# Kernel tuning notes

Hardware: AMD Instinct MI355X
Metric: run time of the kernel (lower is better)

The kernel has to match this reference:

```python
import jax, jax.numpy as jnp
import numpy as np
from jax import lax

D, DIM, FF, V, B, S = 8, 1024, 4096, 32000, 2, 2048
EPS = 1e-6

def _rms(x, w):
    return x * lax.rsqrt(jnp.mean(x * x, axis=-1, keepdims=True) + EPS) * w

def _lin(x, W, b):
    # torch nn.Linear: weight [out, in]
    return x @ W.T + b

def _comb(e1, e2):
    # associative op for h_t = a_t * h_{t-1} + b_t  (h_0 = 0)
    a1, b1 = e1
    a2, b2 = e2
    return a1 * a2, a2 * b1 + b2

def _forward(tokens, emb, h0, Wf, bf, Wi, bi, Wig, big, Wog, bog, n1, n2, Wfc, bfc, Wfa, bfa, Wfo, bfo, nl, Wout, bout):
    # embedding with max_norm=1 renorm semantics
    e = emb[tokens]                                  # [B,S,DIM]
    nrm = jnp.linalg.norm(e, axis=-1, keepdims=True)
    x = jnp.where(nrm > 1.0, e / (nrm + 1e-7), e)
    for i in range(D):
        # --- QuasiLSTM sub-block ---
        x_ = x
        h_in = _rms(x, n1[i])
        f = jax.nn.sigmoid(_lin(h_in, Wf[i], bf[i]))                 # forget gate [B,S,DIM]
        v = jnp.tanh(_lin(h_in, Wi[i], bi[i])) * jax.nn.sigmoid(_lin(h_in, Wig[i], big[i]))
        _, h_inner = lax.associative_scan(_comb, (f, v), axis=1)     # inner-chunk scan (zero init)
        h = h_inner + h0[i][None, None, :] * jnp.cumprod(f, axis=1)  # cross-chunk from last_hidden_init
        y = jnp.tanh(h) * jax.nn.sigmoid(_lin(h_in, Wog[i], bog[i]))
        x = y + x_                                                   # dropout(p) is identity in eval
        # --- SwiGLU FFN sub-block ---
        x_ = x
        z = _rms(x, n2[i])
        u = _lin(z, Wfc[i], bfc[i]) * jax.nn.silu(_lin(z, Wfa[i], bfa[i]))
        x = _lin(u, Wfo[i], bfo[i]) + x_
    x = _rms(x, nl)
    return _lin(x, Wout, bout)                                       # [B,S,V]

def setup_inputs() -> dict:
    key = jax.random.key(0)
    ks = jax.random.split(key, 16)
    n = lambda k, s: jax.random.normal(k, s, jnp.float32) * 0.02
    zD = jnp.zeros((D, DIM), jnp.float32)
    return {
        "tokens": jax.random.randint(ks[0], (B, S), 0, V),
        "emb": n(ks[1], (V, DIM)),
        "h0": jax.random.normal(ks[2], (D, DIM), jnp.float32),
        "Wf": n(ks[3], (D, DIM, DIM)), "bf": zD,
        "Wi": n(ks[4], (D, DIM, DIM)), "bi": zD,
        "Wig": n(ks[5], (D, DIM, DIM)), "big": zD,
        "Wog": n(ks[6], (D, DIM, DIM)), "bog": zD,
        "n1": jnp.ones((D, DIM), jnp.float32),
        "n2": jnp.ones((D, DIM), jnp.float32),
        "Wfc": n(ks[7], (D, FF, DIM)), "bfc": jnp.zeros((D, FF), jnp.float32),
        "Wfa": n(ks[8], (D, FF, DIM)), "bfa": jnp.zeros((D, FF), jnp.float32),
        "Wfo": n(ks[9], (D, DIM, FF)), "bfo": zD,
        "nl": jnp.ones((DIM,), jnp.float32),
        "Wout": n(ks[10], (V, DIM)), "bout": jnp.zeros((V,), jnp.float32),
    }

def reference(tokens, emb, h0, Wf, bf, Wi, bi, Wig, big, Wog, bog, n1, n2, Wfc, bfc, Wfa, bfa, Wfo, bfo, nl, Wout, bout):
    return _forward(tokens, emb, h0, Wf, bf, Wi, bi, Wig, big, Wog, bog, n1, n2, Wfc, bfc, Wfa, bfa, Wfo, bfo, nl, Wout, bout)
```

## Files before the change

### kernel.cpp

```cpp
#include <hip/hip_runtime.h>
#include <hip/hip_bf16.h>
#include <cstdint>
#include <cstddef>

typedef unsigned short u16;
typedef __attribute__((ext_vector_type(4))) float f32x4;
typedef __attribute__((ext_vector_type(8))) short bf16x8;
typedef __attribute__((ext_vector_type(8))) unsigned short u16x8;
typedef __attribute__((ext_vector_type(4))) unsigned short u16x4;

#define D_LAYERS 8
#define DIMN 1024
#define FFD 4096
#define VOCAB 32000
#define MROWS 4096
#define SEQ 2048
#define NCHUNK 64
#define LCHUNK 32

__device__ __forceinline__ u16 f2b(float f) {
  union { float f; unsigned u; } v; v.f = f;
  unsigned r = v.u + 0x7FFFu + ((v.u >> 16) & 1u);
  return (u16)(r >> 16);
}
__device__ __forceinline__ float b2f(u16 h) {
  union { unsigned u; float f; } v; v.u = ((unsigned)h) << 16;
  return v.f;
}
__device__ __forceinline__ float sigm(float x) { return 1.f / (1.f + __expf(-x)); }

__device__ __forceinline__ void async16(const void* g, void* l) {
  auto gp = reinterpret_cast<const __attribute__((address_space(1))) char*>(
      reinterpret_cast<uintptr_t>(g));
  auto lp = reinterpret_cast<__attribute__((address_space(3))) char*>(
      reinterpret_cast<uintptr_t>(l));
  __builtin_amdgcn_global_load_lds(gp, lp, 16, 0, 0);
}

__device__ __forceinline__ float blk_sum(float v) {
  __shared__ float sm[4];
  #pragma unroll
  for (int o = 32; o > 0; o >>= 1) v += __shfl_xor(v, o);
  if ((threadIdx.x & 63) == 0) sm[threadIdx.x >> 6] = v;
  __syncthreads();
  float r = sm[0] + sm[1] + sm[2] + sm[3];
  __syncthreads();
  return r;
}

__global__ __launch_bounds__(256) void k_cvt(const f32x4* __restrict__ in,
                                             u16x8* __restrict__ out) {
  size_t i = (size_t)blockIdx.x * 256 + threadIdx.x;
  f32x4 a = in[i * 2], b = in[i * 2 + 1];
  u16x8 o;
  o[0] = f2b(a[0]); o[1] = f2b(a[1]); o[2] = f2b(a[2]); o[3] = f2b(a[3]);
  o[4] = f2b(b[0]); o[5] = f2b(b[1]); o[6] = f2b(b[2]); o[7] = f2b(b[3]);
  out[i] = o;
}

__global__ __launch_bounds__(256) void k_embed(const int* __restrict__ tok,
                                               const float* __restrict__ emb,
                                               float* __restrict__ x) {
  const int r = blockIdx.x;
  const int tk = tok[r];
  f32x4 v = ((const f32x4*)(emb + (size_t)tk * DIMN))[threadIdx.x];
  float ss = v[0]*v[0] + v[1]*v[1] + v[2]*v[2] + v[3]*v[3];
  float tot = blk_sum(ss);
  float nrm = sqrtf(tot);
  float s = (nrm > 1.f) ? (1.f / (nrm + 1e-7f)) : 1.f;
  f32x4 o = {v[0]*s, v[1]*s, v[2]*s, v[3]*s};
  ((f32x4*)(x + (size_t)r * DIMN))[threadIdx.x] = o;
}

__global__ __launch_bounds__(256) void k_rms(const float* __restrict__ x,
                                             const float* __restrict__ wgt,
                                             u16* __restrict__ out) {
  const int r = blockIdx.x;
  f32x4 v = ((const f32x4*)(x + (size_t)r * DIMN))[threadIdx.x];
  float ss = v[0]*v[0] + v[1]*v[1] + v[2]*v[2] + v[3]*v[3];
  float tot = blk_sum(ss);
  float sc = rsqrtf(tot * (1.f / DIMN) + 1e-6f);
  f32x4 w = ((const f32x4*)wgt)[threadIdx.x];
  u16x4 o;
  o[0] = f2b(v[0] * sc * w[0]);
  o[1] = f2b(v[1] * sc * w[1]);
  o[2] = f2b(v[2] * sc * w[2]);
  o[3] = f2b(v[3] * sc * w[3]);
  ((u16x4*)(out + (size_t)r * DIMN))[threadIdx.x] = o;
}

__global__ __launch_bounds__(256) void k_scanA(const float* __restrict__ f,
                                               const float* __restrict__ ti,
                                               const float* __restrict__ gg,
                                               float* __restrict__ Ac,
                                               float* __restrict__ Vc) {
  const int bx = blockIdx.x;
  const int dg = bx & 3, c = (bx >> 2) & 63, b = bx >> 8;
  const int d = dg * 256 + threadIdx.x;
  const size_t base = ((size_t)(b * SEQ + c * LCHUNK)) * DIMN + d;
  float a = 1.f, h = 0.f;
  #pragma unroll 4
  for (int t = 0; t < LCHUNK; ++t) {
    size_t ix = base + (size_t)t * DIMN;
    float fv = f[ix];
    float vv = ti[ix] * gg[ix];
    h = fv * h + vv;
    a *= fv;
  }
  const size_t ci = ((size_t)(b * NCHUNK + c)) * DIMN + d;
  Ac[ci] = a; Vc[ci] = h;
}

__global__ __launch_bounds__(256) void k_scanB(const float* __restrict__ Ac,
                                               const float* __restrict__ Vc,
                                               const float* __restrict__ h0,
                                               float* __restrict__ carry) {
  const int idx = blockIdx.x * 256 + threadIdx.x;
  const int b = idx >> 10, d = idx & 1023;
  float h = h0[d];
  for (int c = 0; c < NCHUNK; ++c) {
    size_t ci = ((size_t)(b * NCHUNK + c)) * DIMN + d;
    carry[ci] = h;
    h = Ac[ci] * h + Vc[ci];
  }
}

__global__ __launch_bounds__(256) void k_scanC(const float* __restrict__ f,
                                               const float* __restrict__ ti,
                                               const float* __restrict__ gg,
                                               const float* __restrict__ oo,
                                               const float* __restrict__ carry,
                                               float* __restrict__ x) {
  const int bx = blockIdx.x;
  const int dg = bx & 3, c = (bx >> 2) & 63, b = bx >> 8;
  const int d = dg * 256 + threadIdx.x;
  const size_t base = ((size_t)(b * SEQ + c * LCHUNK)) * DIMN + d;
  float h = carry[((size_t)(b * NCHUNK + c)) * DIMN + d];
  for (int t = 0; t < LCHUNK; ++t) {
    size_t ix = base + (size_t)t * DIMN;
    float fv = f[ix];
    h = fv * h + ti[ix] * gg[ix];
    float y = tanhf(h) * oo[ix];
    x[ix] += y;
  }
}

constexpr int EPI_GATES = 0, EPI_SILU_BF = 1, EPI_MUL_BF = 2, EPI_RES_F32 = 3,
              EPI_BIAS_F32 = 4;

template<int BN_T, int EPI>
__global__ __launch_bounds__(256, 2)
void gemm_bt(const u16* __restrict__ A,
             const u16* __restrict__ B0, const u16* __restrict__ B1,
             const u16* __restrict__ B2, const u16* __restrict__ B3,
             const float* __restrict__ bias0, const float* __restrict__ bias1,
             const float* __restrict__ bias2, const float* __restrict__ bias3,
             float* __restrict__ oF0, float* __restrict__ oF1,
             float* __restrict__ oF2, float* __restrict__ oF3,
             u16* __restrict__ oB,
             const u16* __restrict__ exB, const float* __restrict__ exF,
             int N, int K)
{
  constexpr int MF = (BN_T == 128) ? 4 : 2;
  constexpr int WAVES_N = (BN_T == 128) ? 2 : 1;
  constexpr int ISS_B = BN_T / 32;
  __shared__ __align__(16) u16 As[128 * 64];
  __shared__ __align__(16) u16 Bs[BN_T * 64];
  const int tid = threadIdx.x;
  const int w = tid >> 6, lane = tid & 63;
  const int wm = w / WAVES_N, wn = w % WAVES_N;
  const int m0 = blockIdx.x * 128;
  const int n0 = blockIdx.y * BN_T;
  const int z = blockIdx.z;

  const u16* Bw;
  const float* bias;
  float* oF;
  if constexpr (EPI == EPI_GATES) {
    Bw   = (z == 0) ? B0 : (z == 1) ? B1 : (z == 2) ? B2 : B3;
    bias = (z == 0) ? bias0 : (z == 1) ? bias1 : (z == 2) ? bias2 : bias3;
    oF   = (z == 0) ? oF0 : (z == 1) ? oF1 : (z == 2) ? oF2 : oF3;
  } else {
    Bw = B0; bias = bias0; oF = oF0;
  }

  const f32x4 zero = {0.f, 0.f, 0.f, 0.f};
  f32x4 acc[MF][4];
  #pragma unroll
  for (int mf = 0; mf < MF; ++mf)
    #pragma unroll
    for (int nf = 0; nf < 4; ++nf) acc[mf][nf] = zero;

  for (int kt = 0; kt < K; kt += 64) {
    #pragma unroll
    for (int i = 0; i < 4; ++i) {
      int p = i * 4096 + w * 1024 + lane * 16;
      int r = p >> 7;
      int cs = (p & 127) ^ ((r & 7) << 4);
      async16(A + ((size_t)(m0 + r) * K + kt) + (cs >> 1),
              (char*)As + i * 4096 + w * 1024);
    }
    #pragma unroll
    for (int i = 0; i < ISS_B; ++i) {
      int p = i * 4096 + w * 1024 + lane * 16;
      int r = p >> 7;
      int cs = (p & 127) ^ ((r & 7) << 4);
      async16(Bw + ((size_t)(n0 + r) * K + kt) + (cs >> 1),
              (char*)Bs + i * 4096 + w * 1024);
    }
    __syncthreads();
    #pragma unroll
    for (int ks = 0; ks < 2; ++ks) {
      bf16x8 av[MF], bv[4];
      const int cbase = ks * 64 + ((lane >> 4) << 4);
      #pragma unroll
      for (int mf = 0; mf < MF; ++mf) {
        int r = wm * (MF * 16) + mf * 16 + (lane & 15);
        av[mf] = *(const bf16x8*)((const char*)As + r * 128 + (cbase ^ ((r & 7) << 4)));
      }
      #pragma unroll
      for (int nf = 0; nf < 4; ++nf) {
        int r = wn * 64 + nf * 16 + (lane & 15);
        bv[nf] = *(const bf16x8*)((const char*)Bs + r * 128 + (cbase ^ ((r & 7) << 4)));
      }
      #pragma unroll
      for (int mf = 0; mf < MF; ++mf)
        #pragma unroll
        for (int nf = 0; nf < 4; ++nf)
          acc[mf][nf] = __builtin_amdgcn_mfma_f32_16x16x32_bf16(
              av[mf], bv[nf], acc[mf][nf], 0, 0, 0);
    }
    __syncthreads();
  }

  #pragma unroll
  for (int nf = 0; nf < 4; ++nf) {
    const int n = n0 + wn * 64 + nf * 16 + (lane & 15);
    const float bb = bias[n];
    #pragma unroll
    for (int mf = 0; mf < MF; ++mf) {
      #pragma unroll
      for (int j = 0; j < 4; ++j) {
        const int m = m0 + wm * (MF * 16) + mf * 16 + ((lane >> 4) << 2) + j;
        const size_t idx = (size_t)m * N + n;
        float v = acc[mf][nf][j] + bb;
        if constexpr (EPI == EPI_GATES) {
          oF[idx] = (z == 1) ? tanhf(v) : sigm(v);
        } else if constexpr (EPI == EPI_SILU_BF) {
          oB[idx] = f2b(v * sigm(v));
        } else if constexpr (EPI == EPI_MUL_BF) {
          oB[idx] = f2b(v * b2f(exB[idx]));
        } else if constexpr (EPI == EPI_RES_F32) {
          oF[idx] = v + exF[idx];
        } else {
          oF[idx] = v;
        }
      }
    }
  }
}

extern "C" void kernel_launch(void* const* d_in, const int* in_sizes, int n_in,
                              void* d_out, int out_size, void* d_ws, size_t ws_size,
                              hipStream_t stream) {
  (void)in_sizes; (void)n_in; (void)out_size; (void)ws_size;
  const int*   tokens = (const int*)d_in[0];
  const float* emb  = (const float*)d_in[1];
  const float* h0   = (const float*)d_in[2];
  const float* Wf   = (const float*)d_in[3];
  const float* bf_  = (const float*)d_in[4];
  const float* Wi   = (const float*)d_in[5];
  const float* bi_  = (const float*)d_in[6];
  const float* Wig  = (const float*)d_in[7];
  const float* big_ = (const float*)d_in[8];
  const float* Wog  = (const float*)d_in[9];
  const float* bog_ = (const float*)d_in[10];
  const float* n1   = (const float*)d_in[11];
  const float* n2   = (const float*)d_in[12];
  const float* Wfc  = (const float*)d_in[13];
  const float* bfc_ = (const float*)d_in[14];
  const float* Wfa  = (const float*)d_in[15];
  const float* bfa_ = (const float*)d_in[16];
  const float* Wfo  = (const float*)d_in[17];
  const float* bfo_ = (const float*)d_in[18];
  const float* nl_  = (const float*)d_in[19];
  const float* Wout = (const float*)d_in[20];
  const float* bout_= (const float*)d_in[21];
  float* out = (float*)d_out;

  char* p = (char*)d_ws;
  auto alloc = [&](size_t bytes) {
    char* r = p; p += (bytes + 255) & ~(size_t)255; return r;
  };
  u16* wbWf   = (u16*)alloc((size_t)DIMN * DIMN * 2);
  u16* wbWi   = (u16*)alloc((size_t)DIMN * DIMN * 2);
  u16* wbWig  = (u16*)alloc((size_t)DIMN * DIMN * 2);
  u16* wbWog  = (u16*)alloc((size_t)DIMN * DIMN * 2);
  u16* wbWfc  = (u16*)alloc((size_t)FFD * DIMN * 2);
  u16* wbWfa  = (u16*)alloc((size_t)FFD * DIMN * 2);
  u16* wbWfo  = (u16*)alloc((size_t)FFD * DIMN * 2);
  u16* wbWout = (u16*)alloc((size_t)VOCAB * DIMN * 2);
  float* x    = (float*)alloc((size_t)MROWS * DIMN * 4);
  u16* hin    = (u16*)alloc((size_t)MROWS * DIMN * 2);
  float* fbuf = (float*)alloc((size_t)MROWS * DIMN * 4);
  float* tibuf= (float*)alloc((size_t)MROWS * DIMN * 4);
  float* ggbuf= (float*)alloc((size_t)MROWS * DIMN * 4);
  float* oobuf= (float*)alloc((size_t)MROWS * DIMN * 4);
  u16* sa = (u16*)fbuf;
  u16* ub = (u16*)((char*)fbuf + (size_t)MROWS * FFD * 2);
  float* Ac    = (float*)alloc((size_t)2 * NCHUNK * DIMN * 4);
  float* Vc    = (float*)alloc((size_t)2 * NCHUNK * DIMN * 4);
  float* carry = (float*)alloc((size_t)2 * NCHUNK * DIMN * 4);

  auto cvt = [&](const float* src, u16* dst, size_t nelem) {
    k_cvt<<<dim3((unsigned)(nelem / 2048)), dim3(256), 0, stream>>>(
        (const f32x4*)src, (u16x8*)dst);
  };

  k_embed<<<dim3(MROWS), dim3(256), 0, stream>>>(tokens, emb, x);

  for (int L = 0; L < D_LAYERS; ++L) {
    const size_t oDD = (size_t)L * DIMN * DIMN;
    const size_t oFD = (size_t)L * FFD * DIMN;
    cvt(Wf  + oDD, wbWf,  (size_t)DIMN * DIMN);
    cvt(Wi  + oDD, wbWi,  (size_t)DIMN * DIMN);
    cvt(Wig + oDD, wbWig, (size_t)DIMN * DIMN);
    cvt(Wog + oDD, wbWog, (size_t)DIMN * DIMN);
    cvt(Wfc + oFD, wbWfc, (size_t)FFD * DIMN);
    cvt(Wfa + oFD, wbWfa, (size_t)FFD * DIMN);
    cvt(Wfo + oFD, wbWfo, (size_t)FFD * DIMN);

    k_rms<<<dim3(MROWS), dim3(256), 0, stream>>>(x, n1 + (size_t)L * DIMN, hin);

    gemm_bt<128, EPI_GATES><<<dim3(32, 8, 4), dim3(256), 0, stream>>>(
        hin, wbWf, wbWi, wbWig, wbWog,
        bf_ + (size_t)L * DIMN, bi_ + (size_t)L * DIMN,
        big_ + (size_t)L * DIMN, bog_ + (size_t)L * DIMN,
        fbuf, tibuf, ggbuf, oobuf,
        nullptr, nullptr, nullptr, DIMN, DIMN);

    k_scanA<<<dim3(512), dim3(256), 0, stream>>>(fbuf, tibuf, ggbuf, Ac, Vc);
    k_scanB<<<dim3(8), dim3(256), 0, stream>>>(Ac, Vc, h0 + (size_t)L * DIMN, carry);
    k_scanC<<<dim3(512), dim3(256), 0, stream>>>(fbuf, tibuf, ggbuf, oobuf, carry, x);

    k_rms<<<dim3(MROWS), dim3(256), 0, stream>>>(x, n2 + (size_t)L * DIMN, hin);

    gemm_bt<128, EPI_SILU_BF><<<dim3(32, 32, 1), dim3(256), 0, stream>>>(
        hin, wbWfa, nullptr, nullptr, nullptr,
        bfa_ + (size_t)L * FFD, nullptr, nullptr, nullptr,
        nullptr, nullptr, nullptr, nullptr,
        sa, nullptr, nullptr, FFD, DIMN);

    gemm_bt<128, EPI_MUL_BF><<<dim3(32, 32, 1), dim3(256), 0, stream>>>(
        hin, wbWfc, nullptr, nullptr, nullptr,
        bfc_ + (size_t)L * FFD, nullptr, nullptr, nullptr,
        nullptr, nullptr, nullptr, nullptr,
        ub, sa, nullptr, FFD, DIMN);

    gemm_bt<64, EPI_RES_F32><<<dim3(32, 16, 1), dim3(256), 0, stream>>>(
        ub, wbWfo, nullptr, nullptr, nullptr,
        bfo_ + (size_t)L * DIMN, nullptr, nullptr, nullptr,
        x, nullptr, nullptr, nullptr,
        nullptr, nullptr, x, DIMN, FFD);
  }

  cvt(Wout, wbWout, (size_t)VOCAB * DIMN);
  k_rms<<<dim3(MROWS), dim3(256), 0, stream>>>(x, nl_, hin);
  gemm_bt<128, EPI_BIAS_F32><<<dim3(32, 250, 1), dim3(256), 0, stream>>>(
      hin, wbWout, nullptr, nullptr, nullptr,
      bout_, nullptr, nullptr, nullptr,
      out, nullptr, nullptr, nullptr,
      nullptr, nullptr, nullptr, VOCAB, DIMN);
}
```

Baseline: 2.518 ms.

## Add 256x256 double-buffered MFMA GEMM for gates, FFN-up and vocab projections

Introduces a new 512-thread GEMM kernel with 256x256 output tiles and a 128KB double-buffered LDS stage loaded by async copies. It uses a swizzled LDS layout and interleaves loads with MFMA quarter-steps under barriers and priority hints. The four gate weights are packed contiguously so a single N=4096 GEMM computes all gates. The FFN up/gate and vocab GEMMs use the new kernel, and the FFN down GEMM tile is changed from 64 to 128. Larger tiles are meant to raise data reuse and MFMA utilization, at the cost of high LDS use that limits each CU to one block and fewer blocks for the smaller GEMMs.

Result: slower. 2.974 ms (+18.1%).

```diff
diff --git a/kernel.cpp b/kernel.cpp
--- a/kernel.cpp
+++ b/kernel.cpp
@@ -256,6 +256,173 @@
           oF[idx] = v;
         }
       }
+    }
+  }
+}
+
+constexpr int EG4 = 0, ESILU = 1, EMUL = 2, EVOC = 3;
+
+template<int EPI>
+__global__ __launch_bounds__(512, 2)
+void gemm256(const u16* __restrict__ A, const u16* __restrict__ Bm,
+             const float* __restrict__ b0, const float* __restrict__ b1,
+             const float* __restrict__ b2, const float* __restrict__ b3,
+             float* __restrict__ f0, float* __restrict__ f1,
+             float* __restrict__ f2, float* __restrict__ f3,
+             u16* __restrict__ oB, const u16* __restrict__ exB,
+             float* __restrict__ oF,
+             int N, int K, int GX)
+{
+  __shared__ __align__(16) char lds[131072];
+  const int tid = threadIdx.x;
+  const int w = tid >> 6, lane = tid & 63;
+  const int wm = w >> 2, wn = w & 3;
+  const int nwg = gridDim.x, bid = blockIdx.x;
+  const int swz = (bid & 7) * (nwg >> 3) + (bid >> 3);
+  const int m0 = (swz % GX) * 256;
+  const int n0 = (swz / GX) * 256;
+
+  int Dj[8];
+  #pragma unroll
+  for (int j = 0; j < 6; ++j) {
+    const int e = w * 6 + j;
+    Dj[j] = (e < 32) ? (32768 + (e << 10))
+                     : ((((e - 32) >> 3) << 14) + (((e - 32) & 7) << 10));
+  }
+  #pragma unroll
+  for (int j = 0; j < 2; ++j) {
+    const int l = (w << 1) + j;
+    Dj[6 + j] = ((l >> 3) << 14) + 8192 + ((l & 7) << 10);
+  }
+
+  auto issue = [&](int buf, int j, int kt) {
+    const int d = Dj[j];
+    const int qq = d + (lane << 4);
+    const int row = (qq & 32767) >> 7;
+    const int cs = (qq & 127) ^ ((row & 7) << 4);
+    const u16* src = (qq >> 15)
+        ? (Bm + ((size_t)(n0 + row) * K + kt) + (cs >> 1))
+        : (A  + ((size_t)(m0 + row) * K + kt) + (cs >> 1));
+    async16(src, lds + (buf << 16) + d);
+  };
+  auto rdA = [&](int buf, int mf, int ks) -> bf16x8 {
+    const int row = wm * 128 + mf * 16 + (lane & 15);
+    const int col = (ks * 64 + ((lane >> 4) << 4)) ^ ((row & 7) << 4);
+    return *(const bf16x8*)(lds + (buf << 16) + row * 128 + col);
+  };
+  auto rdB = [&](int buf, int nf, int ks) -> bf16x8 {
+    const int row = wn * 64 + nf * 16 + (lane & 15);
+    const int col = (ks * 64 + ((lane >> 4) << 4)) ^ ((row & 7) << 4);
+    return *(const bf16x8*)(lds + (buf << 16) + 32768 + row * 128 + col);
+  };
+
+  const f32x4 zero = {0.f, 0.f, 0.f, 0.f};
+  f32x4 acc[8][4];
+  #pragma unroll
+  for (int mf = 0; mf < 8; ++mf)
+    #pragma unroll
+    for (int nf = 0; nf < 4; ++nf) acc[mf][nf] = zero;
+  bf16x8 av[4][2], bv[2][2];
+
+#define MM256(MFO, NFO)                                                    \
+  __builtin_amdgcn_s_setprio(1);                                           \
+  _Pragma("unroll")                                                        \
+  for (int mf = 0; mf < 4; ++mf)                                           \
+    _Pragma("unroll")                                                      \
+    for (int nf = 0; nf < 2; ++nf)                                         \
+      _Pragma("unroll")                                                    \
+      for (int ks = 0; ks < 2; ++ks)                                       \
+        acc[(MFO) + mf][(NFO) + nf] = __builtin_amdgcn_mfma_f32_16x16x32_bf16( \
+            av[mf][ks], bv[nf][ks], acc[(MFO) + mf][(NFO) + nf], 0, 0, 0); \
+  __builtin_amdgcn_s_setprio(0);
+
+  const int NT = K >> 6;
+  #pragma unroll
+  for (int j = 0; j < 8; ++j) issue(0, j, 0);
+  asm volatile("s_waitcnt vmcnt(2)" ::: "memory");
+  __builtin_amdgcn_s_barrier();
+
+  for (int t = 0; t < NT; ++t) {
+    const int buf = t & 1, nbuf = buf ^ 1;
+    const bool pf = (t + 1 < NT);
+    const int kn = (t + 1) << 6;
+
+    #pragma unroll
+    for (int mf = 0; mf < 4; ++mf) { av[mf][0] = rdA(buf, mf, 0); av[mf][1] = rdA(buf, mf, 1); }
+    #pragma unroll
+    for (int nf = 0; nf < 2; ++nf) { bv[nf][0] = rdB(buf, nf, 0); bv[nf][1] = rdB(buf, nf, 1); }
+    if (pf) { issue(nbuf, 0, kn); issue(nbuf, 1, kn); }
+    __builtin_amdgcn_s_barrier();
+    asm volatile("s_waitcnt lgkmcnt(0)" ::: "memory");
+    MM256(0, 0)
+    __builtin_amdgcn_s_barrier();
+
+    #pragma unroll
+    for (int nf = 0; nf < 2; ++nf) { bv[nf][0] = rdB(buf, 2 + nf, 0); bv[nf][1] = rdB(buf, 2 + nf, 1); }
+    if (pf) { issue(nbuf, 2, kn); issue(nbuf, 3, kn); }
+    __builtin_amdgcn_s_barrier();
+    asm volatile("s_waitcnt lgkmcnt(0)" ::: "memory");
+    MM256(0, 2)
+    if (pf) asm volatile("s_waitcnt vmcnt(4)" ::: "memory");
+    else    asm volatile("s_waitcnt vmcnt(0)" ::: "memory");
+    __builtin_amdgcn_s_barrier();
+
+    #pragma unroll
+    for (int mf = 0; mf < 4; ++mf) { av[mf][0] = rdA(buf, 4 + mf, 0); av[mf][1] = rdA(buf, 4 + mf, 1); }
+    if (pf) { issue(nbuf, 4, kn); issue(nbuf, 5, kn); }
+    __builtin_amdgcn_s_barrier();
+    asm volatile("s_waitcnt lgkmcnt(0)" ::: "memory");
+    MM256(4, 2)
+    __builtin_amdgcn_s_barrier();
+
+    #pragma unroll
+    for (int nf = 0; nf < 2; ++nf) { bv[nf][0] = rdB(buf, nf, 0); bv[nf][1] = rdB(buf, nf, 1); }
+    if (pf) { issue(nbuf, 6, kn); issue(nbuf, 7, kn); }
+    __builtin_amdgcn_s_barrier();
+    asm volatile("s_waitcnt lgkmcnt(0)" ::: "memory");
+    MM256(4, 0)
+    if (pf) asm volatile("s_waitcnt vmcnt(2)" ::: "memory");
+    __builtin_amdgcn_s_barrier();
+  }
+#undef MM256
+
+  if constexpr (EPI == EG4) {
+    const int z = n0 >> 10;
+    const float* bz = (z == 0) ? b0 : (z == 1) ? b1 : (z == 2) ? b2 : b3;
+    float* fz = (z == 0) ? f0 : (z == 1) ? f1 : (z == 2) ? f2 : f3;
+    #pragma unroll
+    for (int nf = 0; nf < 4; ++nf) {
+      const int n = (n0 & 1023) + wn * 64 + nf * 16 + (lane & 15);
+      const float bb = bz[n];
+      #pragma unroll
+      for (int mf = 0; mf < 8; ++mf)
+        #pragma unroll
+        for (int j = 0; j < 4; ++j) {
+          const int m = m0 + wm * 128 + mf * 16 + ((lane >> 4) << 2) + j;
+          float v = acc[mf][nf][j] + bb;
+          fz[(size_t)m * 1024 + n] = (z == 1) ? tanhf(v) : sigm(v);
+        }
+    }
+  } else {
+    #pragma unroll
+    for (int nf = 0; nf < 4; ++nf) {
+      const int n = n0 + wn * 64 + nf * 16 + (lane & 15);
+      const float bb = b0[n];
+      #pragma unroll
+      for (int mf = 0; mf < 8; ++mf)
+        #pragma unroll
+        for (int j = 0; j < 4; ++j) {
+          const int m = m0 + wm * 128 + mf * 16 + ((lane >> 4) << 2) + j;
+          const size_t idx = (size_t)m * N + n;
+          float v = acc[mf][nf][j] + bb;
+          if constexpr (EPI == ESILU) {
+            oB[idx] = f2b(v * sigm(v));
+          } else if constexpr (EPI == EMUL) {
+            oB[idx] = f2b(v * b2f(exB[idx]));
+          } else {
+            oF[idx] = v;
+          }
+        }
     }
   }
 }
@@ -292,10 +459,7 @@
   auto alloc = [&](size_t bytes) {
     char* r = p; p += (bytes + 255) & ~(size_t)255; return r;
   };
-  u16* wbWf   = (u16*)alloc((size_t)DIMN * DIMN * 2);
-  u16* wbWi   = (u16*)alloc((size_t)DIMN * DIMN * 2);
-  u16* wbWig  = (u16*)alloc((size_t)DIMN * DIMN * 2);
-  u16* wbWog  = (u16*)alloc((size_t)DIMN * DIMN * 2);
+  u16* wbGates = (u16*)alloc((size_t)4 * DIMN * DIMN * 2);
   u16* wbWfc  = (u16*)alloc((size_t)FFD * DIMN * 2);
   u16* wbWfa  = (u16*)alloc((size_t)FFD * DIMN * 2);
   u16* wbWfo  = (u16*)alloc((size_t)FFD * DIMN * 2);
@@ -322,22 +486,22 @@
   for (int L = 0; L < D_LAYERS; ++L) {
     const size_t oDD = (size_t)L * DIMN * DIMN;
     const size_t oFD = (size_t)L * FFD * DIMN;
-    cvt(Wf  + oDD, wbWf,  (size_t)DIMN * DIMN);
-    cvt(Wi  + oDD, wbWi,  (size_t)DIMN * DIMN);
-    cvt(Wig + oDD, wbWig, (size_t)DIMN * DIMN);
-    cvt(Wog + oDD, wbWog, (size_t)DIMN * DIMN);
+    cvt(Wf  + oDD, wbGates + (size_t)0 * DIMN * DIMN, (size_t)DIMN * DIMN);
+    cvt(Wi  + oDD, wbGates + (size_t)1 * DIMN * DIMN, (size_t)DIMN * DIMN);
+    cvt(Wig + oDD, wbGates + (size_t)2 * DIMN * DIMN, (size_t)DIMN * DIMN);
+    cvt(Wog + oDD, wbGates + (size_t)3 * DIMN * DIMN, (size_t)DIMN * DIMN);
     cvt(Wfc + oFD, wbWfc, (size_t)FFD * DIMN);
     cvt(Wfa + oFD, wbWfa, (size_t)FFD * DIMN);
     cvt(Wfo + oFD, wbWfo, (size_t)FFD * DIMN);
 
     k_rms<<<dim3(MROWS), dim3(256), 0, stream>>>(x, n1 + (size_t)L * DIMN, hin);
 
-    gemm_bt<128, EPI_GATES><<<dim3(32, 8, 4), dim3(256), 0, stream>>>(
-        hin, wbWf, wbWi, wbWig, wbWog,
+    gemm256<EG4><<<dim3(256), dim3(512), 0, stream>>>(
+        hin, wbGates,
         bf_ + (size_t)L * DIMN, bi_ + (size_t)L * DIMN,
         big_ + (size_t)L * DIMN, bog_ + (size_t)L * DIMN,
         fbuf, tibuf, ggbuf, oobuf,
-        nullptr, nullptr, nullptr, DIMN, DIMN);
+        nullptr, nullptr, nullptr, 4096, DIMN, 16);
 
     k_scanA<<<dim3(512), dim3(256), 0, stream>>>(fbuf, tibuf, ggbuf, Ac, Vc);
     k_scanB<<<dim3(8), dim3(256), 0, stream>>>(Ac, Vc, h0 + (size_t)L * DIMN, carry);
@@ -345,19 +509,19 @@
 
     k_rms<<<dim3(MROWS), dim3(256), 0, stream>>>(x, n2 + (size_t)L * DIMN, hin);
 
-    gemm_bt<128, EPI_SILU_BF><<<dim3(32, 32, 1), dim3(256), 0, stream>>>(
-        hin, wbWfa, nullptr, nullptr, nullptr,
+    gemm256<ESILU><<<dim3(256), dim3(512), 0, stream>>>(
+        hin, wbWfa,
         bfa_ + (size_t)L * FFD, nullptr, nullptr, nullptr,
         nullptr, nullptr, nullptr, nullptr,
-        sa, nullptr, nullptr, FFD, DIMN);
-
-    gemm_bt<128, EPI_MUL_BF><<<dim3(32, 32, 1), dim3(256), 0, stream>>>(
-        hin, wbWfc, nullptr, nullptr, nullptr,
+        sa, nullptr, nullptr, FFD, DIMN, 16);
+
+    gemm256<EMUL><<<dim3(256), dim3(512), 0, stream>>>(
+        hin, wbWfc,
         bfc_ + (size_t)L * FFD, nullptr, nullptr, nullptr,
         nullptr, nullptr, nullptr, nullptr,
-        ub, sa, nullptr, FFD, DIMN);
-
-    gemm_bt<64, EPI_RES_F32><<<dim3(32, 16, 1), dim3(256), 0, stream>>>(
+        ub, sa, nullptr, FFD, DIMN, 16);
+
+    gemm_bt<128, EPI_RES_F32><<<dim3(32, 8), dim3(256), 0, stream>>>(
         ub, wbWfo, nullptr, nullptr, nullptr,
         bfo_ + (size_t)L * DIMN, nullptr, nullptr, nullptr,
         x, nullptr, nullptr, nullptr,
@@ -366,9 +530,9 @@
 
   cvt(Wout, wbWout, (size_t)VOCAB * DIMN);
   k_rms<<<dim3(MROWS), dim3(256), 0, stream>>>(x, nl_, hin);
-  gemm_bt<128, EPI_BIAS_F32><<<dim3(32, 250, 1), dim3(256), 0, stream>>>(
-      hin, wbWout, nullptr, nullptr, nullptr,
+  gemm256<EVOC><<<dim3(2000), dim3(512), 0, stream>>>(
+      hin, wbWout,
       bout_, nullptr, nullptr, nullptr,
-      out, nullptr, nullptr, nullptr,
-      nullptr, nullptr, nullptr, VOCAB, DIMN);
-}
+      nullptr, nullptr, nullptr, nullptr,
+      nullptr, nullptr, out, VOCAB, DIMN, 16);
+}
```

## Fuse paired gate and SwiGLU GEMMs into dual-B kernel, batch weight conversions

Applied to the files above, without the earlier changes.

Adds a dual-output GEMM that shares each A tile across two weight matrices. The tanh input and its sigmoid gate are multiplied in the epilogue, so v is written directly and the scan kernels read one buffer instead of two. The SwiGLU gate and up projections are computed together and written as one bf16 product, removing the intermediate silu buffer round trip and one A reread. The seven per-layer weight conversions merge into one launch, and tanh uses a cheaper exp-based form. The dual kernel uses more LDS and accumulator registers, which may reduce occupancy.

New measurement: 2.139 ms. 1.18x faster.

```diff
diff --git a/kernel.cpp b/kernel.cpp
--- a/kernel.cpp
+++ b/kernel.cpp
@@ -28,6 +28,10 @@
   return v.f;
 }
 __device__ __forceinline__ float sigm(float x) { return 1.f / (1.f + __expf(-x)); }
+__device__ __forceinline__ float ftanh(float x) {
+  float e = __expf(2.f * x);
+  return 1.f - 2.f / (e + 1.f);
+}
 
 __device__ __forceinline__ void async16(const void* g, void* l) {
   auto gp = reinterpret_cast<const __attribute__((address_space(1))) char*>(
@@ -56,6 +60,39 @@
   o[0] = f2b(a[0]); o[1] = f2b(a[1]); o[2] = f2b(a[2]); o[3] = f2b(a[3]);
   o[4] = f2b(b[0]); o[5] = f2b(b[1]); o[6] = f2b(b[2]); o[7] = f2b(b[3]);
   out[i] = o;
+}
+
+__global__ __launch_bounds__(256) void k_cvt7(
+    const float* __restrict__ Wf, const float* __restrict__ Wi,
+    const float* __restrict__ Wig, const float* __restrict__ Wog,
+    const float* __restrict__ Wfc, const float* __restrict__ Wfa,
+    const float* __restrict__ Wfo,
+    u16* __restrict__ dGates,
+    u16* __restrict__ dFc, u16* __restrict__ dFa, u16* __restrict__ dFo,
+    int L)
+{
+  const int b = blockIdx.x;
+  const float* src; u16* dst; size_t off;
+  if (b < 2048) {
+    const int g = b >> 9, r = b & 511;
+    const float* s = (g == 0) ? Wf : (g == 1) ? Wi : (g == 2) ? Wig : Wog;
+    src = s + (size_t)L * 1048576;
+    dst = dGates + (size_t)g * 1048576;
+    off = (size_t)r * 2048;
+  } else if (b < 4096) {
+    src = Wfc + (size_t)L * 4194304; dst = dFc; off = (size_t)(b - 2048) * 2048;
+  } else if (b < 6144) {
+    src = Wfa + (size_t)L * 4194304; dst = dFa; off = (size_t)(b - 4096) * 2048;
+  } else {
+    src = Wfo + (size_t)L * 4194304; dst = dFo; off = (size_t)(b - 6144) * 2048;
+  }
+  const size_t i = off + (size_t)threadIdx.x * 8;
+  f32x4 a = *(const f32x4*)(src + i);
+  f32x4 c = *(const f32x4*)(src + i + 4);
+  u16x8 o;
+  o[0] = f2b(a[0]); o[1] = f2b(a[1]); o[2] = f2b(a[2]); o[3] = f2b(a[3]);
+  o[4] = f2b(c[0]); o[5] = f2b(c[1]); o[6] = f2b(c[2]); o[7] = f2b(c[3]);
+  *(u16x8*)(dst + i) = o;
 }
 
 __global__ __launch_bounds__(256) void k_embed(const int* __restrict__ tok,
@@ -90,8 +127,7 @@
 }
 
 __global__ __launch_bounds__(256) void k_scanA(const float* __restrict__ f,
-                                               const float* __restrict__ ti,
-                                               const float* __restrict__ gg,
+                                               const float* __restrict__ v,
                                                float* __restrict__ Ac,
                                                float* __restrict__ Vc) {
   const int bx = blockIdx.x;
@@ -103,8 +139,7 @@
   for (int t = 0; t < LCHUNK; ++t) {
     size_t ix = base + (size_t)t * DIMN;
     float fv = f[ix];
-    float vv = ti[ix] * gg[ix];
-    h = fv * h + vv;
+    h = fv * h + v[ix];
     a *= fv;
   }
   const size_t ci = ((size_t)(b * NCHUNK + c)) * DIMN + d;
@@ -126,8 +161,7 @@
 }
 
 __global__ __launch_bounds__(256) void k_scanC(const float* __restrict__ f,
-                                               const float* __restrict__ ti,
-                                               const float* __restrict__ gg,
+                                               const float* __restrict__ v,
                                                const float* __restrict__ oo,
                                                const float* __restrict__ carry,
                                                float* __restrict__ x) {
@@ -139,24 +173,19 @@
   for (int t = 0; t < LCHUNK; ++t) {
     size_t ix = base + (size_t)t * DIMN;
     float fv = f[ix];
-    h = fv * h + ti[ix] * gg[ix];
-    float y = tanhf(h) * oo[ix];
-    x[ix] += y;
-  }
-}
-
-constexpr int EPI_GATES = 0, EPI_SILU_BF = 1, EPI_MUL_BF = 2, EPI_RES_F32 = 3,
-              EPI_BIAS_F32 = 4;
+    h = fv * h + v[ix];
+    x[ix] += ftanh(h) * oo[ix];
+  }
+}
+
+constexpr int EPI_SILU_BF = 1, EPI_MUL_BF = 2, EPI_RES_F32 = 3, EPI_BIAS_F32 = 4;
 
 template<int BN_T, int EPI>
 __global__ __launch_bounds__(256, 2)
 void gemm_bt(const u16* __restrict__ A,
-             const u16* __restrict__ B0, const u16* __restrict__ B1,
-             const u16* __restrict__ B2, const u16* __restrict__ B3,
-             const float* __restrict__ bias0, const float* __restrict__ bias1,
-             const float* __restrict__ bias2, const float* __restrict__ bias3,
-             float* __restrict__ oF0, float* __restrict__ oF1,
-             float* __restrict__ oF2, float* __restrict__ oF3,
+             const u16* __restrict__ B0,
+             const float* __restrict__ bias0,
+             float* __restrict__ oF0,
              u16* __restrict__ oB,
              const u16* __restrict__ exB, const float* __restrict__ exF,
              int N, int K)
@@ -171,18 +200,10 @@
   const int wm = w / WAVES_N, wn = w % WAVES_N;
   const int m0 = blockIdx.x * 128;
   const int n0 = blockIdx.y * BN_T;
-  const int z = blockIdx.z;
-
-  const u16* Bw;
-  const float* bias;
-  float* oF;
-  if constexpr (EPI == EPI_GATES) {
-    Bw   = (z == 0) ? B0 : (z == 1) ? B1 : (z == 2) ? B2 : B3;
-    bias = (z == 0) ? bias0 : (z == 1) ? bias1 : (z == 2) ? bias2 : bias3;
-    oF   = (z == 0) ? oF0 : (z == 1) ? oF1 : (z == 2) ? oF2 : oF3;
-  } else {
-    Bw = B0; bias = bias0; oF = oF0;
-  }
+
+  const u16* Bw = B0;
+  const float* bias = bias0;
+  float* oF = oF0;
 
   const f32x4 zero = {0.f, 0.f, 0.f, 0.f};
   f32x4 acc[MF][4];
@@ -244,9 +265,7 @@
         const int m = m0 + wm * (MF * 16) + mf * 16 + ((lane >> 4) << 2) + j;
         const size_t idx = (size_t)m * N + n;
         float v = acc[mf][nf][j] + bb;
-        if constexpr (EPI == EPI_GATES) {
-          oF[idx] = (z == 1) ? tanhf(v) : sigm(v);
-        } else if constexpr (EPI == EPI_SILU_BF) {
+        if constexpr (EPI == EPI_SILU_BF) {
           oB[idx] = f2b(v * sigm(v));
         } else if constexpr (EPI == EPI_MUL_BF) {
           oB[idx] = f2b(v * b2f(exB[idx]));
@@ -254,6 +273,112 @@
           oF[idx] = v + exF[idx];
         } else {
           oF[idx] = v;
+        }
+      }
+    }
+  }
+}
+
+constexpr int EDG = 0, EDF = 1;
+
+template<int EPI>
+__global__ __launch_bounds__(256, 2)
+void gemm_dual(const u16* __restrict__ A,
+               const u16* __restrict__ Ba0, const u16* __restrict__ Bb0,
+               const u16* __restrict__ Ba1, const u16* __restrict__ Bb1,
+               const float* __restrict__ ba0, const float* __restrict__ bb0,
+               const float* __restrict__ ba1, const float* __restrict__ bb1,
+               float* __restrict__ oV,
+               float* __restrict__ oFa, float* __restrict__ oFb,
+               u16* __restrict__ oU,
+               int N, int K)
+{
+  __shared__ __align__(16) u16 As[128 * 64];
+  __shared__ __align__(16) u16 Bsa[128 * 64];
+  __shared__ __align__(16) u16 Bsb[128 * 64];
+  const int tid = threadIdx.x;
+  const int w = tid >> 6, lane = tid & 63;
+  const int wm = w >> 1, wn = w & 1;
+  const int m0 = blockIdx.x * 128;
+  const int n0 = blockIdx.y * 128;
+  const int z = blockIdx.z;
+
+  const u16* Ba = (EPI == EDG && z) ? Ba1 : Ba0;
+  const u16* Bb = (EPI == EDG && z) ? Bb1 : Bb0;
+  const float* ba = (EPI == EDG && z) ? ba1 : ba0;
+  const float* bb = (EPI == EDG && z) ? bb1 : bb0;
+
+  const f32x4 zero = {0.f, 0.f, 0.f, 0.f};
+  f32x4 accA[4][4], accB[4][4];
+  #pragma unroll
+  for (int mf = 0; mf < 4; ++mf)
+    #pragma unroll
+    for (int nf = 0; nf < 4; ++nf) { accA[mf][nf] = zero; accB[mf][nf] = zero; }
+
+  for (int kt = 0; kt < K; kt += 64) {
+    #pragma unroll
+    for (int i = 0; i < 4; ++i) {
+      const int p = i * 4096 + w * 1024 + lane * 16;
+      const int r = p >> 7;
+      const int cs = (p & 127) ^ ((r & 7) << 4);
+      async16(A  + ((size_t)(m0 + r) * K + kt) + (cs >> 1),
+              (char*)As + i * 4096 + w * 1024);
+      async16(Ba + ((size_t)(n0 + r) * K + kt) + (cs >> 1),
+              (char*)Bsa + i * 4096 + w * 1024);
+      async16(Bb + ((size_t)(n0 + r) * K + kt) + (cs >> 1),
+              (char*)Bsb + i * 4096 + w * 1024);
+    }
+    __syncthreads();
+    #pragma unroll
+    for (int ks = 0; ks < 2; ++ks) {
+      bf16x8 av[4], bva[4], bvb[4];
+      const int cbase = ks * 64 + ((lane >> 4) << 4);
+      #pragma unroll
+      for (int mf = 0; mf < 4; ++mf) {
+        const int r = wm * 64 + mf * 16 + (lane & 15);
+        av[mf] = *(const bf16x8*)((const char*)As + r * 128 + (cbase ^ ((r & 7) << 4)));
+      }
+      #pragma unroll
+      for (int nf = 0; nf < 4; ++nf) {
+        const int r = wn * 64 + nf * 16 + (lane & 15);
+        const int off = r * 128 + (cbase ^ ((r & 7) << 4));
+        bva[nf] = *(const bf16x8*)((const char*)Bsa + off);
+        bvb[nf] = *(const bf16x8*)((const char*)Bsb + off);
+      }
+      #pragma unroll
+      for (int mf = 0; mf < 4; ++mf)
+        #pragma unroll
+        for (int nf = 0; nf < 4; ++nf) {
+          accA[mf][nf] = __builtin_amdgcn_mfma_f32_16x16x32_bf16(
+              av[mf], bva[nf], accA[mf][nf], 0, 0, 0);
+          accB[mf][nf] = __builtin_amdgcn_mfma_f32_16x16x32_bf16(
+              av[mf], bvb[nf], accB[mf][nf], 0, 0, 0);
+        }
+    }
+    __syncthreads();
+  }
+
+  #pragma unroll
+  for (int nf = 0; nf < 4; ++nf) {
+    const int n = n0 + wn * 64 + nf * 16 + (lane & 15);
+    const float bba = ba[n], bbb = bb[n];
+    #pragma unroll
+    for (int mf = 0; mf < 4; ++mf) {
+      #pragma unroll
+      for (int j = 0; j < 4; ++j) {
+        const int m = m0 + wm * 64 + mf * 16 + ((lane >> 4) << 2) + j;
+        const size_t idx = (size_t)m * N + n;
+        const float va = accA[mf][nf][j] + bba;
+        const float vb = accB[mf][nf][j] + bbb;
+        if constexpr (EPI == EDG) {
+          if (z == 0) {
+            oV[idx] = ftanh(va) * sigm(vb);
+          } else {
+            oFa[idx] = sigm(va);
+            oFb[idx] = sigm(vb);
+          }
+        } else {
+          oU[idx] = f2b(vb * va * sigm(va));
         }
       }
     }
@@ -292,10 +417,7 @@
   auto alloc = [&](size_t bytes) {
     char* r = p; p += (bytes + 255) & ~(size_t)255; return r;
   };
-  u16* wbWf   = (u16*)alloc((size_t)DIMN * DIMN * 2);
-  u16* wbWi   = (u16*)alloc((size_t)DIMN * DIMN * 2);
-  u16* wbWig  = (u16*)alloc((size_t)DIMN * DIMN * 2);
-  u16* wbWog  = (u16*)alloc((size_t)DIMN * DIMN * 2);
+  u16* wbGates = (u16*)alloc((size_t)4 * DIMN * DIMN * 2);
   u16* wbWfc  = (u16*)alloc((size_t)FFD * DIMN * 2);
   u16* wbWfa  = (u16*)alloc((size_t)FFD * DIMN * 2);
   u16* wbWfo  = (u16*)alloc((size_t)FFD * DIMN * 2);
@@ -303,72 +425,54 @@
   float* x    = (float*)alloc((size_t)MROWS * DIMN * 4);
   u16* hin    = (u16*)alloc((size_t)MROWS * DIMN * 2);
   float* fbuf = (float*)alloc((size_t)MROWS * DIMN * 4);
-  float* tibuf= (float*)alloc((size_t)MROWS * DIMN * 4);
-  float* ggbuf= (float*)alloc((size_t)MROWS * DIMN * 4);
+  float* vbuf = (float*)alloc((size_t)MROWS * DIMN * 4);
   float* oobuf= (float*)alloc((size_t)MROWS * DIMN * 4);
-  u16* sa = (u16*)fbuf;
-  u16* ub = (u16*)((char*)fbuf + (size_t)MROWS * FFD * 2);
+  u16* ub     = (u16*)alloc((size_t)MROWS * FFD * 2);
   float* Ac    = (float*)alloc((size_t)2 * NCHUNK * DIMN * 4);
   float* Vc    = (float*)alloc((size_t)2 * NCHUNK * DIMN * 4);
   float* carry = (float*)alloc((size_t)2 * NCHUNK * DIMN * 4);
 
-  auto cvt = [&](const float* src, u16* dst, size_t nelem) {
-    k_cvt<<<dim3((unsigned)(nelem / 2048)), dim3(256), 0, stream>>>(
-        (const f32x4*)src, (u16x8*)dst);
-  };
+  u16* wbWf  = wbGates;
+  u16* wbWi  = wbGates + (size_t)1 * DIMN * DIMN;
+  u16* wbWig = wbGates + (size_t)2 * DIMN * DIMN;
+  u16* wbWog = wbGates + (size_t)3 * DIMN * DIMN;
 
   k_embed<<<dim3(MROWS), dim3(256), 0, stream>>>(tokens, emb, x);
 
   for (int L = 0; L < D_LAYERS; ++L) {
-    const size_t oDD = (size_t)L * DIMN * DIMN;
-    const size_t oFD = (size_t)L * FFD * DIMN;
-    cvt(Wf  + oDD, wbWf,  (size_t)DIMN * DIMN);
-    cvt(Wi  + oDD, wbWi,  (size_t)DIMN * DIMN);
-    cvt(Wig + oDD, wbWig, (size_t)DIMN * DIMN);
-    cvt(Wog + oDD, wbWog, (size_t)DIMN * DIMN);
-    cvt(Wfc + oFD, wbWfc, (size_t)FFD * DIMN);
-    cvt(Wfa + oFD, wbWfa, (size_t)FFD * DIMN);
-    cvt(Wfo + oFD, wbWfo, (size_t)FFD * DIMN);
+    k_cvt7<<<dim3(8192), dim3(256), 0, stream>>>(
+        Wf, Wi, Wig, Wog, Wfc, Wfa, Wfo,
+        wbGates, wbWfc, wbWfa, wbWfo, L);
 
     k_rms<<<dim3(MROWS), dim3(256), 0, stream>>>(x, n1 + (size_t)L * DIMN, hin);
 
-    gemm_bt<128, EPI_GATES><<<dim3(32, 8, 4), dim3(256), 0, stream>>>(
-        hin, wbWf, wbWi, wbWig, wbWog,
-        bf_ + (size_t)L * DIMN, bi_ + (size_t)L * DIMN,
-        big_ + (size_t)L * DIMN, bog_ + (size_t)L * DIMN,
-        fbuf, tibuf, ggbuf, oobuf,
-        nullptr, nullptr, nullptr, DIMN, DIMN);
-
-    k_scanA<<<dim3(512), dim3(256), 0, stream>>>(fbuf, tibuf, ggbuf, Ac, Vc);
+    gemm_dual<EDG><<<dim3(32, 8, 2), dim3(256), 0, stream>>>(
+        hin, wbWi, wbWig, wbWf, wbWog,
+        bi_ + (size_t)L * DIMN, big_ + (size_t)L * DIMN,
+        bf_ + (size_t)L * DIMN, bog_ + (size_t)L * DIMN,
+        vbuf, fbuf, oobuf, nullptr, DIMN, DIMN);
+
+    k_scanA<<<dim3(512), dim3(256), 0, stream>>>(fbuf, vbuf, Ac, Vc);
     k_scanB<<<dim3(8), dim3(256), 0, stream>>>(Ac, Vc, h0 + (size_t)L * DIMN, carry);
-    k_scanC<<<dim3(512), dim3(256), 0, stream>>>(fbuf, tibuf, ggbuf, oobuf, carry, x);
+    k_scanC<<<dim3(512), dim3(256), 0, stream>>>(fbuf, vbuf, oobuf, carry, x);
 
     k_rms<<<dim3(MROWS), dim3(256), 0, stream>>>(x, n2 + (size_t)L * DIMN, hin);
 
-    gemm_bt<128, EPI_SILU_BF><<<dim3(32, 32, 1), dim3(256), 0, stream>>>(
-        hin, wbWfa, nullptr, nullptr, nullptr,
-        bfa_ + (size_t)L * FFD, nullptr, nullptr, nullptr,
-        nullptr, nullptr, nullptr, nullptr,
-        sa, nullptr, nullptr, FFD, DIMN);
-
-    gemm_bt<128, EPI_MUL_BF><<<dim3(32, 32, 1), dim3(256), 0, stream>>>(
-        hin, wbWfc, nullptr, nullptr, nullptr,
-        bfc_ + (size_t)L * FFD, nullptr, nullptr, nullptr,
-        nullptr, nullptr, nullptr, nullptr,
-        ub, sa, nullptr, FFD, DIMN);
-
-    gemm_bt<64, EPI_RES_F32><<<dim3(32, 16, 1), dim3(256), 0, stream>>>(
-        ub, wbWfo, nullptr, nullptr, nullptr,
-        bfo_ + (size_t)L * DIMN, nullptr, nullptr, nullptr,
-        x, nullptr, nullptr, nullptr,
-        nullptr, nullptr, x, DIMN, FFD);
-  }
-
-  cvt(Wout, wbWout, (size_t)VOCAB * DIMN);
+    gemm_dual<EDF><<<dim3(32, 32, 1), dim3(256), 0, stream>>>(
+        hin, wbWfa, wbWfc, nullptr, nullptr,
+        bfa_ + (size_t)L * FFD, bfc_ + (size_t)L * FFD, nullptr, nullptr,
+        nullptr, nullptr, nullptr, ub, FFD, DIMN);
+
+    gemm_bt<64, EPI_RES_F32><<<dim3(32, 16), dim3(256), 0, stream>>>(
+        ub, wbWfo,
+        bfo_ + (size_t)L * DIMN,
+        x, nullptr, nullptr, x, DIMN, FFD);
+  }
+
+  k_cvt<<<dim3(16000), dim3(256), 0, stream>>>((const f32x4*)Wout, (u16x8*)wbWout);
   k_rms<<<dim3(MROWS), dim3(256), 0, stream>>>(x, nl_, hin);
-  gemm_bt<128, EPI_BIAS_F32><<<dim3(32, 250, 1), dim3(256), 0, stream>>>(
-      hin, wbWout, nullptr, nullptr, nullptr,
-      bout_, nullptr, nullptr, nullptr,
-      out, nullptr, nullptr, nullptr,
-      nullptr, nullptr, nullptr, VOCAB, DIMN);
-}
+  gemm_bt<128, EPI_BIAS_F32><<<dim3(32, 250), dim3(256), 0, stream>>>(
+      hin, wbWout,
+      bout_,
+      out, nullptr, nullptr, nullptr, VOCAB, DIMN);
+}
```
